# Kernel optimization log

Hardware: AMD Instinct MI355X
Metric: run time of the kernel (lower is better)

## Reference

```python
import jax, jax.numpy as jnp
import numpy as np

NUM_HEADS = 16
HIDDEN = 2048
HEAD_SIZE = HIDDEN // NUM_HEADS        # 128
ROTARY_PCT = 0.25
ROTARY_DIM = int(HEAD_SIZE * ROTARY_PCT)  # 32
ROTARY_BASE = 10000.0
BATCH = 4
SEQ = 1024
TOTAL = BATCH * SEQ


def setup_inputs() -> dict:
    key = jax.random.key(0)
    k1, k2, k3 = jax.random.split(key, 3)
    hidden_states = jax.random.normal(k1, (TOTAL, HIDDEN), dtype=jnp.float32)
    w_qkv = jax.random.normal(k2, (3 * HIDDEN, HIDDEN), dtype=jnp.float32) * (HIDDEN ** -0.5)
    b_qkv = jnp.zeros((3 * HIDDEN,), dtype=jnp.float32)
    w_dense = jax.random.normal(k3, (HIDDEN, HIDDEN), dtype=jnp.float32) * (HIDDEN ** -0.5)
    b_dense = jnp.zeros((HIDDEN,), dtype=jnp.float32)
    layer_past = jnp.zeros((TOTAL, 2, NUM_HEADS, HEAD_SIZE), dtype=jnp.float32)
    position_ids = jnp.tile(jnp.arange(SEQ, dtype=jnp.int64), BATCH)
    cu_seqlens = (jnp.arange(BATCH + 1, dtype=jnp.int32) * SEQ)
    return {
        "hidden_states": hidden_states, "layer_past": layer_past,
        "w_qkv": w_qkv, "b_qkv": b_qkv, "w_dense": w_dense, "b_dense": b_dense,
        "position_ids": position_ids, "cu_seqlens": cu_seqlens,
        "max_s": SEQ, "prefill": 1,
    }


def _apply_rotary(x, cos, sin):
    # x: [T, h, d]; GPT-NeoX (rotate-half, non-interleaved) on first ROTARY_DIM dims
    x_rot, x_pass = x[..., :ROTARY_DIM], x[..., ROTARY_DIM:]
    half = ROTARY_DIM // 2
    x1, x2 = x_rot[..., :half], x_rot[..., half:]
    return jnp.concatenate([x1 * cos - x2 * sin, x1 * sin + x2 * cos, x_pass], axis=-1)


def reference(hidden_states, layer_past, w_qkv, b_qkv, w_dense, b_dense,
              position_ids, cu_seqlens, max_s, prefill):
    # QKV projection: [T, 3H]
    qkv = hidden_states @ w_qkv.T + b_qkv
    # rearrange '... (h three d)' then permute -> [T, 3, h, d]
    qkv = qkv.reshape(TOTAL, NUM_HEADS, 3, HEAD_SIZE).transpose(0, 2, 1, 3)

    # rotary cos/sin per token position: [T, 1, ROTARY_DIM/2]
    inv_freq = 1.0 / (ROTARY_BASE ** (jnp.arange(0, ROTARY_DIM, 2, dtype=jnp.float32) / ROTARY_DIM))
    freqs = position_ids.astype(jnp.float32)[:, None] * inv_freq[None, :]
    cos = jnp.cos(freqs)[:, None, :]
    sin = jnp.sin(freqs)[:, None, :]

    q = _apply_rotary(qkv[:, 0], cos, sin)   # [T, h, d]
    k = _apply_rotary(qkv[:, 1], cos, sin)
    v = qkv[:, 2]

    # prefill: cache write layer_past[...] = kv_rot (byproduct, not returned here)
    # ragged causal flash attention; all sequences have equal length SEQ here
    qb = q.reshape(BATCH, SEQ, NUM_HEADS, HEAD_SIZE)
    kb = k.reshape(BATCH, SEQ, NUM_HEADS, HEAD_SIZE)
    vb = v.reshape(BATCH, SEQ, NUM_HEADS, HEAD_SIZE)

    scale = HEAD_SIZE ** -0.5
    scores = jnp.einsum('bqhd,bkhd->bhqk', qb, kb) * scale  # [B, h, S, S]
    causal = jnp.tril(jnp.ones((SEQ, SEQ), dtype=bool))
    scores = jnp.where(causal[None, None], scores, jnp.finfo(scores.dtype).min)
    probs = jax.nn.softmax(scores, axis=-1)
    attn = jnp.einsum('bhqk,bkhd->bqhd', probs, vb)          # [B, S, h, d]
    attn = attn.reshape(TOTAL, HIDDEN)

    return attn @ w_dense.T + b_dense
```

## Files before the change

kernel.cpp:

```cpp
#include <hip/hip_runtime.h>
#include <stdint.h>

#define NUM_HEADS 16
#define HIDDEN    2048
#define HEAD_SIZE 128
#define TOTAL     4096
#define SEQ       1024
#define QKV_N     (3*HIDDEN)

typedef __bf16 bf16x8 __attribute__((ext_vector_type(8)));
typedef float  f32x4  __attribute__((ext_vector_type(4)));

__device__ __forceinline__ unsigned short f2bf(float f) {
  unsigned u = __float_as_uint(f);
  u += 0x7FFFu + ((u >> 16) & 1u);
  return (unsigned short)(u >> 16);
}
__device__ __forceinline__ float bf2f(unsigned short h) {
  return __uint_as_float(((unsigned)h) << 16);
}
__device__ __forceinline__ void cp16(void* lds, const void* g) {
  __builtin_amdgcn_global_load_lds(
      (const __attribute__((address_space(1))) void*)g,
      (__attribute__((address_space(3))) void*)lds, 16, 0, 0);
}

__global__ __launch_bounds__(256) void f32_to_bf16_k(
    const float* __restrict__ in, unsigned short* __restrict__ out, int n)
{
  int i = (blockIdx.x * 256 + threadIdx.x) * 4;
  if (i >= n) return;
  float4 v = *(const float4*)(in + i);
  unsigned p0 = (unsigned)f2bf(v.x) | ((unsigned)f2bf(v.y) << 16);
  unsigned p1 = (unsigned)f2bf(v.z) | ((unsigned)f2bf(v.w) << 16);
  uint2 pk; pk.x = p0; pk.y = p1;
  *(uint2*)(out + i) = pk;
}

template <int MODE>
__global__ __launch_bounds__(256) void gemm_bt(
    const unsigned short* __restrict__ A,
    const unsigned short* __restrict__ B,
    const float* __restrict__ bias,
    float* __restrict__ Cf,
    unsigned short* __restrict__ Qb,
    unsigned short* __restrict__ Kb,
    unsigned short* __restrict__ Vt,
    int M, int N, int K)
{
  __shared__ unsigned short lsA[128*32];
  __shared__ unsigned short lsB[128*32];
  const int tid  = threadIdx.x;
  const int w    = tid >> 6, lane = tid & 63;
  const int quad = lane >> 4, lm = lane & 15;
  const int wm   = w & 1, wn = w >> 1;
  const int mBase = blockIdx.y * 128;
  const int nBase = blockIdx.x * 128;
  const int swz = (lm >> 1) & 3;

  const f32x4 zero4 = {0.f, 0.f, 0.f, 0.f};
  f32x4 acc[4][4];
#pragma unroll
  for (int i = 0; i < 4; i++)
#pragma unroll
    for (int j = 0; j < 4; j++) acc[i][j] = zero4;

  const int cg = ((tid & 3) ^ ((tid >> 3) & 3)) * 16;

  for (int k0 = 0; k0 < K; k0 += 32) {
#pragma unroll
    for (int i = 0; i < 2; i++) {
      int off = i * 4096 + tid * 16;
      int row = off >> 6;
      cp16((char*)lsA + off, (const char*)(A + (size_t)(mBase + row) * K + k0) + cg);
    }
#pragma unroll
    for (int i = 0; i < 2; i++) {
      int off = i * 4096 + tid * 16;
      int row = off >> 6;
      cp16((char*)lsB + off, (const char*)(B + (size_t)(nBase + row) * K + k0) + cg);
    }
    __syncthreads();
    bf16x8 af[4], bfr[4];
#pragma unroll
    for (int mf = 0; mf < 4; mf++)
      af[mf] = *(const bf16x8*)(lsA + (wm * 64 + mf * 16 + lm) * 32 + (quad ^ swz) * 8);
#pragma unroll
    for (int nf = 0; nf < 4; nf++)
      bfr[nf] = *(const bf16x8*)(lsB + (wn * 64 + nf * 16 + lm) * 32 + (quad ^ swz) * 8);
#pragma unroll
    for (int mf = 0; mf < 4; mf++)
#pragma unroll
      for (int nf = 0; nf < 4; nf++)
        acc[mf][nf] = __builtin_amdgcn_mfma_f32_16x16x32_bf16(af[mf], bfr[nf], acc[mf][nf], 0, 0, 0);
    __syncthreads();
  }

#pragma unroll
  for (int nf = 0; nf < 4; nf++) {
    int col = nBase + wn * 64 + nf * 16 + lm;
    float bv = bias[col];
    if (MODE == 0) {
#pragma unroll
      for (int mf = 0; mf < 4; mf++) {
        int row0 = mBase + wm * 64 + mf * 16 + quad * 4;
#pragma unroll
        for (int r = 0; r < 4; r++)
          Cf[(size_t)(row0 + r) * N + col] = acc[mf][nf][r] + bv;
      }
    } else {
      int chunk = col >> 7;
      int hh = chunk / 3, t = chunk - 3 * hh;
      int d = col & 127;
      if (t == 2) {
#pragma unroll
        for (int mf = 0; mf < 4; mf++) {
          int row0 = mBase + wm * 64 + mf * 16 + quad * 4;
          int b = row0 >> 10, s0 = row0 & 1023;
          unsigned u0 = (unsigned)f2bf(acc[mf][nf][0] + bv) | ((unsigned)f2bf(acc[mf][nf][1] + bv) << 16);
          unsigned u1 = (unsigned)f2bf(acc[mf][nf][2] + bv) | ((unsigned)f2bf(acc[mf][nf][3] + bv) << 16);
          uint2 pk; pk.x = u0; pk.y = u1;
          *(uint2*)(Vt + ((size_t)(b * NUM_HEADS + hh) * HEAD_SIZE + d) * SEQ + s0) = pk;
        }
      } else {
        unsigned short* dst = (t == 0) ? Qb : Kb;
#pragma unroll
        for (int mf = 0; mf < 4; mf++) {
          int row0 = mBase + wm * 64 + mf * 16 + quad * 4;
#pragma unroll
          for (int r = 0; r < 4; r++) {
            int row = row0 + r;
            int b = row >> 10, s = row & 1023;
            dst[((size_t)(b * NUM_HEADS + hh) * SEQ + s) * HEAD_SIZE + d] = f2bf(acc[mf][nf][r] + bv);
          }
        }
      }
    }
  }
}

__global__ __launch_bounds__(256) void rotary_k(
    unsigned short* __restrict__ Qb, unsigned short* __restrict__ Kb,
    const int* __restrict__ pos_ids)
{
  int f = blockIdx.x * 256 + threadIdx.x;
  int qk   = f >> 20;
  int rem  = f & 0xFFFFF;
  int bh   = rem >> 14;
  int rem2 = rem & 0x3FFF;
  int s    = rem2 >> 4;
  int i    = rem2 & 15;
  int b    = bh >> 4;
  float pos = (float)pos_ids[b * SEQ + s];
  float inv = exp2f(-0.8304820237f * (float)i);
  float ang = pos * inv, sn, c;
  sincosf(ang, &sn, &c);
  unsigned short* p = (qk ? Kb : Qb) + ((size_t)bh * SEQ + s) * HEAD_SIZE;
  float x1 = bf2f(p[i]);
  float x2 = bf2f(p[i + 16]);
  p[i]      = f2bf(x1 * c - x2 * sn);
  p[i + 16] = f2bf(x1 * sn + x2 * c);
}

__global__ __launch_bounds__(256, 2) void flash_attn_k(
    const unsigned short* __restrict__ Q,
    const unsigned short* __restrict__ K,
    const unsigned short* __restrict__ VT,
    unsigned short* __restrict__ O)
{
  const int bh = blockIdx.x;
  const int pair = blockIdx.y;
  const int qa = 15 - pair, qb = pair;
  const int b = bh >> 4, h = bh & 15;
  const size_t base = (size_t)bh * SEQ * HEAD_SIZE;
  const unsigned short* Qp = Q + base;
  const unsigned short* Kp = K + base;
  const unsigned short* Vp = VT + base;

  __shared__ unsigned short Ks[2][4][64*32];
  __shared__ unsigned short Vl[2][128*64];
  __shared__ unsigned short Ps[64][72];

  const int tid  = threadIdx.x;
  const int w    = tid >> 6, lane = tid & 63;
  const int quad = lane >> 4, lm = lane & 15;
  const int swz4 = (lm >> 1) & 3;
  const int swz8 = lm & 7;
  const int cgK = ((tid & 3) ^ ((tid >> 3) & 3)) * 8;
  const int cgV = ((tid & 7) ^ ((tid >> 3) & 7)) * 8;

  const float K1 = 0.1275156876f;
  const f32x4 zero4 = {0.f, 0.f, 0.f, 0.f};
  const __bf16 one = (__bf16)1.0f;
  const bf16x8 vones = {one, one, one, one, one, one, one, one};

  auto stage = [&](int buf, int kt) {
    const unsigned short* krow = Kp + (size_t)(kt * 64 + (tid >> 2)) * HEAD_SIZE + cgK;
#pragma unroll
    for (int kk = 0; kk < 4; kk++)
      cp16((char*)&Ks[buf][kk][0] + tid * 16, krow + kk * 32);
#pragma unroll
    for (int i = 0; i < 4; i++) {
      int off = i * 4096 + tid * 16;
      int d = off >> 7;
      cp16((char*)&Vl[buf][0] + off, Vp + (size_t)d * SEQ + kt * 64 + cgV);
    }
  };

  int buf = 0;
  stage(0, 0);

  for (int ph = 0; ph < 2; ph++) {
    const int qt = ph ? qb : qa;
    bf16x8 qf[4];
    {
      const unsigned short* qrow = Qp + (size_t)(qt * 64 + w * 16 + lm) * HEAD_SIZE;
#pragma unroll
      for (int kk = 0; kk < 4; kk++)
        qf[kk] = *(const bf16x8*)(qrow + kk * 32 + quad * 8);
    }
    float m_r[4];
#pragma unroll
    for (int r = 0; r < 4; r++) m_r[r] = -1e30f;
    f32x4 lacc = zero4;
    f32x4 o[8];
#pragma unroll
    for (int i = 0; i < 8; i++) o[i] = zero4;

    for (int kt = 0; kt <= qt; ++kt) {
      __syncthreads();
      bool last = (ph == 1) && (kt == qt);
      if (!last) stage(buf ^ 1, (kt < qt) ? kt + 1 : 0);

      f32x4 sf[4];
#pragma unroll
      for (int nf = 0; nf < 4; nf++) {
        f32x4 accs = zero4;
#pragma unroll
        for (int kk = 0; kk < 4; kk++) {
          bf16x8 kfrag = *(const bf16x8*)(&Ks[buf][kk][(nf * 16 + lm) * 32 + (quad ^ swz4) * 8]);
          accs = __builtin_amdgcn_mfma_f32_16x16x32_bf16(qf[kk], kfrag, accs, 0, 0, 0);
        }
        sf[nf] = accs;
      }
      if (kt == qt) {
        int qrow0 = qt * 64 + w * 16 + quad * 4;
#pragma unroll
        for (int nf = 0; nf < 4; nf++) {
          int col = kt * 64 + nf * 16 + lm;
#pragma unroll
          for (int r = 0; r < 4; r++)
            if (col > qrow0 + r) sf[nf][r] = -1e30f;
        }
      }
      float alpha[4];
#pragma unroll
      for (int r = 0; r < 4; r++) {
        float v = fmaxf(fmaxf(sf[0][r], sf[1][r]), fmaxf(sf[2][r], sf[3][r]));
        v = fmaxf(v, __shfl_xor(v, 1));
        v = fmaxf(v, __shfl_xor(v, 2));
        v = fmaxf(v, __shfl_xor(v, 4));
        v = fmaxf(v, __shfl_xor(v, 8));
        float mn = fmaxf(m_r[r], v);
        alpha[r] = exp2f((m_r[r] - mn) * K1);
        m_r[r] = mn;
      }
#pragma unroll
      for (int nf = 0; nf < 4; nf++)
#pragma unroll
        for (int r = 0; r < 4; r++) {
          float p = exp2f((sf[nf][r] - m_r[r]) * K1);
          Ps[w * 16 + quad * 4 + r][nf * 16 + lm] = f2bf(p);
        }
#pragma unroll
      for (int df = 0; df < 8; df++)
#pragma unroll
        for (int r = 0; r < 4; r++) o[df][r] *= alpha[r];
#pragma unroll
      for (int r = 0; r < 4; r++) lacc[r] *= alpha[r];

#pragma unroll
      for (int ks = 0; ks < 2; ks++) {
        bf16x8 pf = *(const bf16x8*)(&Ps[w * 16 + lm][ks * 32 + quad * 8]);
        lacc = __builtin_amdgcn_mfma_f32_16x16x32_bf16(pf, vones, lacc, 0, 0, 0);
#pragma unroll
        for (int df = 0; df < 8; df++) {
          bf16x8 vf = *(const bf16x8*)(&Vl[buf][(df * 16 + lm) * 64 + (((ks * 4 + quad) ^ swz8)) * 8]);
          o[df] = __builtin_amdgcn_mfma_f32_16x16x32_bf16(pf, vf, o[df], 0, 0, 0);
        }
      }
      buf ^= 1;
    }

    float rl[4];
#pragma unroll
    for (int r = 0; r < 4; r++) rl[r] = 1.f / lacc[r];
    int row0 = b * SEQ + qt * 64 + w * 16 + quad * 4;
#pragma unroll
    for (int df = 0; df < 8; df++) {
      int col = h * HEAD_SIZE + df * 16 + lm;
#pragma unroll
      for (int r = 0; r < 4; r++)
        O[(size_t)(row0 + r) * HIDDEN + col] = f2bf(o[df][r] * rl[r]);
    }
  }
}

extern "C" void kernel_launch(void* const* d_in, const int* in_sizes, int n_in,
                              void* d_out, int out_size, void* d_ws, size_t ws_size,
                              hipStream_t stream)
{
  const float* hs   = (const float*)d_in[0];
  const float* wqkv = (const float*)d_in[2];
  const float* bqkv = (const float*)d_in[3];
  const float* wd   = (const float*)d_in[4];
  const float* bd   = (const float*)d_in[5];
  const int*   pos  = (const int*)d_in[6];

  char* ws = (char*)d_ws;
  unsigned short* hsb = (unsigned short*)ws;  ws += (size_t)TOTAL * HIDDEN * 2;
  unsigned short* wqb = (unsigned short*)ws;  ws += (size_t)QKV_N * HIDDEN * 2;
  unsigned short* wdb = (unsigned short*)ws;  ws += (size_t)HIDDEN * HIDDEN * 2;
  unsigned short* Qb  = (unsigned short*)ws;  ws += (size_t)TOTAL * HIDDEN * 2;
  unsigned short* Kb  = (unsigned short*)ws;  ws += (size_t)TOTAL * HIDDEN * 2;
  unsigned short* Vt  = (unsigned short*)ws;  ws += (size_t)TOTAL * HIDDEN * 2;
  unsigned short* attnb = hsb;
  if (ws_size < (size_t)(ws - (char*)d_ws)) return;

  f32_to_bf16_k<<<TOTAL * HIDDEN / 1024, 256, 0, stream>>>(hs, hsb, TOTAL * HIDDEN);
  f32_to_bf16_k<<<QKV_N * HIDDEN / 1024, 256, 0, stream>>>(wqkv, wqb, QKV_N * HIDDEN);
  f32_to_bf16_k<<<HIDDEN * HIDDEN / 1024, 256, 0, stream>>>(wd, wdb, HIDDEN * HIDDEN);

  gemm_bt<1><<<dim3(QKV_N / 128, TOTAL / 128), 256, 0, stream>>>(
      hsb, wqb, bqkv, nullptr, Qb, Kb, Vt, TOTAL, QKV_N, HIDDEN);

  rotary_k<<<(2 * 64 * SEQ * 16) / 256, 256, 0, stream>>>(Qb, Kb, pos);

  flash_attn_k<<<dim3(64, 8), 256, 0, stream>>>(Qb, Kb, Vt, attnb);

  gemm_bt<0><<<dim3(HIDDEN / 128, TOTAL / 128), 256, 0, stream>>>(
      attnb, wdb, bd, (float*)d_out, nullptr, nullptr, nullptr, TOTAL, HIDDEN, HIDDEN);
}
```

Before: 410.8 us.

## Fuse rotary into QKV GEMM epilogue, double-buffer GEMM LDS, merge conversions

Three separate changes. The three f32-to-bf16 conversion launches are merged into one launch, and the rotary embedding is applied inside the QKV GEMM epilogue, which removes the separate rotary kernel and its read-modify-write pass over Q and K. The GEMM main loop now double-buffers its LDS tiles, issuing the next k-slice's async loads before the MFMAs and dropping one barrier per iteration. This costs twice the LDS per block and adds per-row sincos work to the epilogue.

```diff
diff --git a/kernel.cpp b/kernel.cpp
--- a/kernel.cpp
+++ b/kernel.cpp
@@ -25,16 +25,21 @@
       (__attribute__((address_space(3))) void*)lds, 16, 0, 0);
 }
 
-__global__ __launch_bounds__(256) void f32_to_bf16_k(
-    const float* __restrict__ in, unsigned short* __restrict__ out, int n)
+__global__ __launch_bounds__(256) void f32_to_bf16_multi(
+    const float* __restrict__ a, unsigned short* __restrict__ oa, int na,
+    const float* __restrict__ b, unsigned short* __restrict__ ob, int nb,
+    const float* __restrict__ c, unsigned short* __restrict__ oc, int nc)
 {
   int i = (blockIdx.x * 256 + threadIdx.x) * 4;
-  if (i >= n) return;
-  float4 v = *(const float4*)(in + i);
+  const float* src; unsigned short* dst;
+  if (i < na)            { src = a; dst = oa; }
+  else if (i < na + nb)  { i -= na; src = b; dst = ob; }
+  else                   { i -= na + nb; if (i >= nc) return; src = c; dst = oc; }
+  float4 v = *(const float4*)(src + i);
   unsigned p0 = (unsigned)f2bf(v.x) | ((unsigned)f2bf(v.y) << 16);
   unsigned p1 = (unsigned)f2bf(v.z) | ((unsigned)f2bf(v.w) << 16);
   uint2 pk; pk.x = p0; pk.y = p1;
-  *(uint2*)(out + i) = pk;
+  *(uint2*)(dst + i) = pk;
 }
 
 template <int MODE>
@@ -42,14 +47,15 @@
     const unsigned short* __restrict__ A,
     const unsigned short* __restrict__ B,
     const float* __restrict__ bias,
+    const int* __restrict__ pos_ids,
     float* __restrict__ Cf,
     unsigned short* __restrict__ Qb,
     unsigned short* __restrict__ Kb,
     unsigned short* __restrict__ Vt,
     int M, int N, int K)
 {
-  __shared__ unsigned short lsA[128*32];
-  __shared__ unsigned short lsB[128*32];
+  __shared__ unsigned short lsA[2][128*32];
+  __shared__ unsigned short lsB[2][128*32];
   const int tid  = threadIdx.x;
   const int w    = tid >> 6, lane = tid & 63;
   const int quad = lane >> 4, lm = lane & 15;
@@ -66,41 +72,49 @@
     for (int j = 0; j < 4; j++) acc[i][j] = zero4;
 
   const int cg = ((tid & 3) ^ ((tid >> 3) & 3)) * 16;
-
-  for (int k0 = 0; k0 < K; k0 += 32) {
+  const int srow = tid >> 2;
+
+  auto stage = [&](int bufi, int k0) {
 #pragma unroll
     for (int i = 0; i < 2; i++) {
       int off = i * 4096 + tid * 16;
       int row = off >> 6;
-      cp16((char*)lsA + off, (const char*)(A + (size_t)(mBase + row) * K + k0) + cg);
+      cp16((char*)&lsA[bufi][0] + off, (const char*)(A + (size_t)(mBase + row) * K + k0) + cg);
     }
 #pragma unroll
     for (int i = 0; i < 2; i++) {
       int off = i * 4096 + tid * 16;
       int row = off >> 6;
-      cp16((char*)lsB + off, (const char*)(B + (size_t)(nBase + row) * K + k0) + cg);
-    }
+      cp16((char*)&lsB[bufi][0] + off, (const char*)(B + (size_t)(nBase + row) * K + k0) + cg);
+    }
+  };
+
+  int buf = 0;
+  stage(0, 0);
+
+  for (int k0 = 0; k0 < K; k0 += 32) {
     __syncthreads();
     bf16x8 af[4], bfr[4];
 #pragma unroll
     for (int mf = 0; mf < 4; mf++)
-      af[mf] = *(const bf16x8*)(lsA + (wm * 64 + mf * 16 + lm) * 32 + (quad ^ swz) * 8);
+      af[mf] = *(const bf16x8*)(&lsA[buf][(wm * 64 + mf * 16 + lm) * 32 + (quad ^ swz) * 8]);
 #pragma unroll
     for (int nf = 0; nf < 4; nf++)
-      bfr[nf] = *(const bf16x8*)(lsB + (wn * 64 + nf * 16 + lm) * 32 + (quad ^ swz) * 8);
+      bfr[nf] = *(const bf16x8*)(&lsB[buf][(wn * 64 + nf * 16 + lm) * 32 + (quad ^ swz) * 8]);
+    if (k0 + 32 < K) stage(buf ^ 1, k0 + 32);
 #pragma unroll
     for (int mf = 0; mf < 4; mf++)
 #pragma unroll
       for (int nf = 0; nf < 4; nf++)
         acc[mf][nf] = __builtin_amdgcn_mfma_f32_16x16x32_bf16(af[mf], bfr[nf], acc[mf][nf], 0, 0, 0);
-    __syncthreads();
+    buf ^= 1;
   }
 
-#pragma unroll
-  for (int nf = 0; nf < 4; nf++) {
-    int col = nBase + wn * 64 + nf * 16 + lm;
-    float bv = bias[col];
-    if (MODE == 0) {
+  if (MODE == 0) {
+#pragma unroll
+    for (int nf = 0; nf < 4; nf++) {
+      int col = nBase + wn * 64 + nf * 16 + lm;
+      float bv = bias[col];
 #pragma unroll
       for (int mf = 0; mf < 4; mf++) {
         int row0 = mBase + wm * 64 + mf * 16 + quad * 4;
@@ -108,11 +122,18 @@
         for (int r = 0; r < 4; r++)
           Cf[(size_t)(row0 + r) * N + col] = acc[mf][nf][r] + bv;
       }
-    } else {
-      int chunk = col >> 7;
-      int hh = chunk / 3, t = chunk - 3 * hh;
-      int d = col & 127;
-      if (t == 2) {
+    }
+  } else {
+    const int col0 = nBase + wn * 64;
+    const int chunk = col0 >> 7;
+    const int hh = chunk / 3, t = chunk - 3 * hh;
+    const bool lower = ((col0 >> 6) & 1) == 0;
+    if (t == 2) {
+#pragma unroll
+      for (int nf = 0; nf < 4; nf++) {
+        int col = col0 + nf * 16 + lm;
+        float bv = bias[col];
+        int d = col & 127;
 #pragma unroll
         for (int mf = 0; mf < 4; mf++) {
           int row0 = mBase + wm * 64 + mf * 16 + quad * 4;
@@ -122,8 +143,13 @@
           uint2 pk; pk.x = u0; pk.y = u1;
           *(uint2*)(Vt + ((size_t)(b * NUM_HEADS + hh) * HEAD_SIZE + d) * SEQ + s0) = pk;
         }
-      } else {
-        unsigned short* dst = (t == 0) ? Qb : Kb;
+      }
+    } else {
+      unsigned short* dst = (t == 0) ? Qb : Kb;
+      if (lower) {
+        const float inv = exp2f(-0.8304820237f * (float)lm);
+        const float bv0 = bias[col0 + lm];
+        const float bv1 = bias[col0 + 16 + lm];
 #pragma unroll
         for (int mf = 0; mf < 4; mf++) {
           int row0 = mBase + wm * 64 + mf * 16 + quad * 4;
@@ -131,35 +157,50 @@
           for (int r = 0; r < 4; r++) {
             int row = row0 + r;
             int b = row >> 10, s = row & 1023;
-            dst[((size_t)(b * NUM_HEADS + hh) * SEQ + s) * HEAD_SIZE + d] = f2bf(acc[mf][nf][r] + bv);
+            float pos = (float)pos_ids[row];
+            float sn, cs;
+            sincosf(pos * inv, &sn, &cs);
+            float x1 = acc[mf][0][r] + bv0;
+            float x2 = acc[mf][1][r] + bv1;
+            size_t rb = ((size_t)(b * NUM_HEADS + hh) * SEQ + s) * HEAD_SIZE;
+            dst[rb + lm]      = f2bf(x1 * cs - x2 * sn);
+            dst[rb + 16 + lm] = f2bf(x1 * sn + x2 * cs);
           }
         }
+#pragma unroll
+        for (int nf = 2; nf < 4; nf++) {
+          float bv = bias[col0 + nf * 16 + lm];
+          int d = nf * 16 + lm;
+#pragma unroll
+          for (int mf = 0; mf < 4; mf++) {
+            int row0 = mBase + wm * 64 + mf * 16 + quad * 4;
+#pragma unroll
+            for (int r = 0; r < 4; r++) {
+              int row = row0 + r;
+              int b = row >> 10, s = row & 1023;
+              dst[((size_t)(b * NUM_HEADS + hh) * SEQ + s) * HEAD_SIZE + d] = f2bf(acc[mf][nf][r] + bv);
+            }
+          }
+        }
+      } else {
+#pragma unroll
+        for (int nf = 0; nf < 4; nf++) {
+          float bv = bias[col0 + nf * 16 + lm];
+          int d = 64 + nf * 16 + lm;
+#pragma unroll
+          for (int mf = 0; mf < 4; mf++) {
+            int row0 = mBase + wm * 64 + mf * 16 + quad * 4;
+#pragma unroll
+            for (int r = 0; r < 4; r++) {
+              int row = row0 + r;
+              int b = row >> 10, s = row & 1023;
+              dst[((size_t)(b * NUM_HEADS + hh) * SEQ + s) * HEAD_SIZE + d] = f2bf(acc[mf][nf][r] + bv);
+            }
+          }
+        }
       }
     }
   }
-}
-
-__global__ __launch_bounds__(256) void rotary_k(
-    unsigned short* __restrict__ Qb, unsigned short* __restrict__ Kb,
-    const int* __restrict__ pos_ids)
-{
-  int f = blockIdx.x * 256 + threadIdx.x;
-  int qk   = f >> 20;
-  int rem  = f & 0xFFFFF;
-  int bh   = rem >> 14;
-  int rem2 = rem & 0x3FFF;
-  int s    = rem2 >> 4;
-  int i    = rem2 & 15;
-  int b    = bh >> 4;
-  float pos = (float)pos_ids[b * SEQ + s];
-  float inv = exp2f(-0.8304820237f * (float)i);
-  float ang = pos * inv, sn, c;
-  sincosf(ang, &sn, &c);
-  unsigned short* p = (qk ? Kb : Qb) + ((size_t)bh * SEQ + s) * HEAD_SIZE;
-  float x1 = bf2f(p[i]);
-  float x2 = bf2f(p[i + 16]);
-  p[i]      = f2bf(x1 * c - x2 * sn);
-  p[i + 16] = f2bf(x1 * sn + x2 * c);
 }
 
 __global__ __launch_bounds__(256, 2) void flash_attn_k(
@@ -327,17 +368,15 @@
   unsigned short* attnb = hsb;
   if (ws_size < (size_t)(ws - (char*)d_ws)) return;
 
-  f32_to_bf16_k<<<TOTAL * HIDDEN / 1024, 256, 0, stream>>>(hs, hsb, TOTAL * HIDDEN);
-  f32_to_bf16_k<<<QKV_N * HIDDEN / 1024, 256, 0, stream>>>(wqkv, wqb, QKV_N * HIDDEN);
-  f32_to_bf16_k<<<HIDDEN * HIDDEN / 1024, 256, 0, stream>>>(wd, wdb, HIDDEN * HIDDEN);
+  const int na = TOTAL * HIDDEN, nb = QKV_N * HIDDEN, nc = HIDDEN * HIDDEN;
+  f32_to_bf16_multi<<<(na + nb + nc) / 1024, 256, 0, stream>>>(
+      hs, hsb, na, wqkv, wqb, nb, wd, wdb, nc);
 
   gemm_bt<1><<<dim3(QKV_N / 128, TOTAL / 128), 256, 0, stream>>>(
-      hsb, wqb, bqkv, nullptr, Qb, Kb, Vt, TOTAL, QKV_N, HIDDEN);
-
-  rotary_k<<<(2 * 64 * SEQ * 16) / 256, 256, 0, stream>>>(Qb, Kb, pos);
+      hsb, wqb, bqkv, pos, nullptr, Qb, Kb, Vt, TOTAL, QKV_N, HIDDEN);
 
   flash_attn_k<<<dim3(64, 8), 256, 0, stream>>>(Qb, Kb, Vt, attnb);
 
   gemm_bt<0><<<dim3(HIDDEN / 128, TOTAL / 128), 256, 0, stream>>>(
-      attnb, wdb, bd, (float*)d_out, nullptr, nullptr, nullptr, TOTAL, HIDDEN, HIDDEN);
-}
+      attnb, wdb, bd, pos, (float*)d_out, nullptr, nullptr, nullptr, TOTAL, HIDDEN, HIDDEN);
+}
```

New measurement: 386.3 us. -6.0%, faster.
